# Kernel optimization log

Measured on AMD Instinct MI355X. Metric: run time of the kernel, lower is better.

The kernel has to match this reference:

```python
import jax, jax.numpy as jnp
import numpy as np

BIG = 1e9
EPS_BETA = 1e-6
EPS_BN = 1e-5

N_NODES = 50000
N_EDGES = 800000
IN_DIM = 128
OUT_DIM = 128


def setup_inputs() -> dict:
    key = jax.random.key(0)
    ks = jax.random.split(key, 8)
    h = jax.random.normal(ks[0], (N_NODES, IN_DIM), dtype=jnp.float32)
    src = jax.random.randint(ks[1], (N_EDGES,), 0, N_NODES, dtype=jnp.int32)
    dst = jax.random.randint(ks[2], (N_EDGES,), 0, N_NODES, dtype=jnp.int32)
    sigma_GD = jax.random.uniform(ks[3], (N_EDGES,), dtype=jnp.float32)
    fc_w = jax.random.normal(ks[4], (IN_DIM, OUT_DIM), dtype=jnp.float32) / np.sqrt(IN_DIM)
    fc_b = jax.random.normal(ks[5], (OUT_DIM,), dtype=jnp.float32) * 0.01
    attn_w = jax.random.normal(ks[6], (2 * OUT_DIM, 1), dtype=jnp.float32) / np.sqrt(2 * OUT_DIM)
    attn_b = jax.random.normal(ks[7], (1,), dtype=jnp.float32) * 0.01
    bn_gamma = jnp.ones((OUT_DIM,), dtype=jnp.float32)
    bn_beta = jnp.zeros((OUT_DIM,), dtype=jnp.float32)
    return {"h": h, "src": src, "dst": dst, "sigma_GD": sigma_GD,
            "fc_w": fc_w, "fc_b": fc_b, "attn_w": attn_w, "attn_b": attn_b,
            "bn_gamma": bn_gamma, "bn_beta": bn_beta}


def reference(h, src, dst, sigma_GD, fc_w, fc_b, attn_w, attn_b, bn_gamma, bn_beta):
    n = h.shape[0]
    # node projection
    z = h @ fc_w + fc_b                                   # [N, D]
    z = jnp.where(jnp.isinf(z), BIG, z)
    # per-edge attention logits: concat(src,dst) @ W == src@W1 + dst@W2 (avoid concat materialization)
    d = z.shape[1]
    w_src, w_dst = attn_w[:d], attn_w[d:]
    z_src = z[src]                                        # [E, D]
    a = z_src @ w_src + z[dst] @ w_dst + attn_b           # [E, 1]
    a = jnp.where(jnp.isinf(a), BIG, a)
    e = jax.nn.leaky_relu(a, negative_slope=0.01)[:, 0]   # [E]
    # segment softmax over incoming edges (mailbox softmax)
    m = jax.ops.segment_max(e, dst, num_segments=n)       # [N]
    ex = jnp.exp(e - m[dst])
    denom = jax.ops.segment_sum(ex, dst, num_segments=n)  # [N]
    alpha = ex / denom[dst]                               # [E]
    # beta: sigma_GD normalized per destination node
    bsum = jax.ops.segment_sum(sigma_GD, dst, num_segments=n)
    beta = sigma_GD / (bsum[dst] + EPS_BETA)              # [E]
    # weighted scatter-sum of source features
    h_new = jax.ops.segment_sum((alpha * beta)[:, None] * z_src, dst, num_segments=n)  # [N, D]
    h_new = jnp.where(jnp.isinf(h_new), BIG, h_new)
    # BatchNorm1d (training-mode batch stats, biased variance, as torch does)
    mu = h_new.mean(axis=0)
    var = ((h_new - mu) ** 2).mean(axis=0)
    h_bn = (h_new - mu) * jax.lax.rsqrt(var + EPS_BN) * bn_gamma + bn_beta
    return jax.nn.elu(h_bn)
```

## Files before the change

kernel.cpp:

```cpp
#include <hip/hip_runtime.h>
#include <hip/hip_fp16.h>
#include <math.h>

#define N_NODES 50000
#define N_EDGES 800000
#define BIGV 1000000000.0f
#define NBLK_GEMM 3125
#define CHUNK 1024
#define NCHUNK 782
#define NBUCKET 782
#define NB4 784
#define BMAX 1280
#define NBLK_BN 512

typedef _Float16 half8 __attribute__((ext_vector_type(8)));
typedef float floatx4 __attribute__((ext_vector_type(4)));

__device__ __forceinline__ float clampinf(float x) { return isinf(x) ? BIGV : x; }

__device__ __forceinline__ void barrier_lgkm_only() {
    __builtin_amdgcn_sched_barrier(0);
    asm volatile("s_waitcnt lgkmcnt(0)" ::: "memory");
    __builtin_amdgcn_s_barrier();
    __builtin_amdgcn_sched_barrier(0);
}

__global__ __launch_bounds__(256) void k_prep(const float* __restrict__ W,
                                              __half* __restrict__ wt,
                                              const int* __restrict__ dst,
                                              int* __restrict__ countsT)
{
    __shared__ int hist[NB4];
    const int t = threadIdx.x;
    const int idx = blockIdx.x * 256 + t;
    if (idx < 16384) {
        int n = idx >> 7, k = idx & 127;
        wt[idx] = __float2half(W[k * 128 + n]);
    }
    for (int i = t; i < NB4; i += 256) hist[i] = 0;
    __syncthreads();
    const int base = blockIdx.x * CHUNK;
    for (int i = t; i < CHUNK; i += 256) {
        int e = base + i;
        if (e < N_EDGES) atomicAdd(&hist[dst[e] >> 6], 1);
    }
    __syncthreads();
    for (int i = t; i < NB4; i += 256)
        countsT[i * NB4 + blockIdx.x] = hist[i];
}

__global__ __launch_bounds__(256) void k_off(const int* __restrict__ countsT,
                                             int* __restrict__ cursC,
                                             int* __restrict__ btot)
{
    const int wv = (blockIdx.x << 2) + (threadIdx.x >> 6);
    const int l = threadIdx.x & 63;
    if (wv >= NBUCKET) {
        if (l == 0 && wv < NB4) btot[wv] = 0;
        return;
    }
    const int* row = countsT + (size_t)wv * NB4;
    int carry = 0;
    #pragma unroll
    for (int p = 0; p < 13; ++p) {
        const int c = p * 64 + l;
        const int v = (c < NCHUNK) ? row[c] : 0;
        int x = v;
        #pragma unroll
        for (int o = 1; o < 64; o <<= 1) {
            int u = __shfl_up(x, o);
            if (l >= o) x += u;
        }
        if (c < NCHUNK) cursC[(size_t)c * NB4 + wv] = carry + x - v;
        carry += __shfl(x, 63);
    }
    if (l == 0) btot[wv] = carry;
}

__global__ __launch_bounds__(256) void k_gemm(
    const float* __restrict__ h, const __half* __restrict__ wt,
    const float* __restrict__ bias, const float* __restrict__ attn_w,
    __half* __restrict__ zh, float* __restrict__ sv, float* __restrict__ tv)
{
    __shared__ _Float16 hA[16][136];
    __shared__ float spart[4][16], tpart[4][16];

    const int tid = threadIdx.x;
    const int lane = tid & 63;
    const int wv = tid >> 6;
    const int l16 = lane & 15;
    const int oct = lane >> 4;
    const int n0 = wv << 5;
    const int node0 = blockIdx.x << 4;

    {
        const float4* h4 = (const float4*)(h + (size_t)node0 * 128);
        for (int i = tid; i < 512; i += 256) {
            int r = i >> 5, c4 = i & 31;
            float4 v = h4[i];
            union { __half2 h2[2]; uint2 u; } pk;
            pk.h2[0] = __floats2half2_rn(v.x, v.y);
            pk.h2[1] = __floats2half2_rn(v.z, v.w);
            *(uint2*)&hA[r][c4 << 2] = pk.u;
        }
    }

    half8 bfrag[4][2];
    #pragma unroll
    for (int kk = 0; kk < 4; ++kk)
        #pragma unroll
        for (int t = 0; t < 2; ++t)
            bfrag[kk][t] = *(const half8*)(wt + (size_t)(n0 + t * 16 + l16) * 128
                                              + kk * 32 + oct * 8);

    const float bv0 = bias[n0 + l16],         bv1 = bias[n0 + 16 + l16];
    const float ws0 = attn_w[n0 + l16],       ws1 = attn_w[n0 + 16 + l16];
    const float wd0 = attn_w[128 + n0 + l16], wd1 = attn_w[128 + n0 + 16 + l16];

    barrier_lgkm_only();

    floatx4 acc0 = {0.f, 0.f, 0.f, 0.f};
    floatx4 acc1 = {0.f, 0.f, 0.f, 0.f};
    #pragma unroll
    for (int kk = 0; kk < 4; ++kk) {
        half8 a = *(const half8*)&hA[l16][(kk << 5) + (oct << 3)];
        acc0 = __builtin_amdgcn_mfma_f32_16x16x32_f16(a, bfrag[kk][0], acc0, 0, 0, 0);
        acc1 = __builtin_amdgcn_mfma_f32_16x16x32_f16(a, bfrag[kk][1], acc1, 0, 0, 0);
    }

    float s_acc[4], t_acc[4];
    #pragma unroll
    for (int r = 0; r < 4; ++r) {
        float z0 = clampinf(acc0[r] + bv0);
        float z1 = clampinf(acc1[r] + bv1);
        const int row = (oct << 2) + r;
        zh[(size_t)(node0 + row) * 128 + n0 + l16]      = __float2half(z0);
        zh[(size_t)(node0 + row) * 128 + n0 + 16 + l16] = __float2half(z1);
        s_acc[r] = z0 * ws0 + z1 * ws1;
        t_acc[r] = z0 * wd0 + z1 * wd1;
    }
    #pragma unroll
    for (int r = 0; r < 4; ++r) {
        #pragma unroll
        for (int o = 1; o < 16; o <<= 1) {
            s_acc[r] += __shfl_xor(s_acc[r], o);
            t_acc[r] += __shfl_xor(t_acc[r], o);
        }
    }
    if (l16 == 0) {
        #pragma unroll
        for (int r = 0; r < 4; ++r) {
            spart[wv][(oct << 2) + r] = s_acc[r];
            tpart[wv][(oct << 2) + r] = t_acc[r];
        }
    }
    barrier_lgkm_only();
    if (tid < 16) {
        sv[node0 + tid] = spart[0][tid] + spart[1][tid] + spart[2][tid] + spart[3][tid];
        tv[node0 + tid] = tpart[0][tid] + tpart[1][tid] + tpart[2][tid] + tpart[3][tid];
    }
}

__global__ __launch_bounds__(256) void k_scat(
    const int* __restrict__ src, const int* __restrict__ dst,
    const float* __restrict__ sigma,
    const float* __restrict__ sv, const float* __restrict__ tv,
    const float* __restrict__ attn_b,
    const int* __restrict__ cursC, const int* __restrict__ btot,
    float4* __restrict__ tmp, int* __restrict__ bbase_g)
{
    __shared__ int cur[NB4];
    __shared__ int bb[NB4];
    __shared__ int tsc[256];
    const int t = threadIdx.x;
    const int self = blockIdx.x;

    for (int i = t; i < NB4; i += 256) cur[i] = cursC[(size_t)self * NB4 + i];

    uint4 bt = {0u, 0u, 0u, 0u};
    int tsum = 0;
    if (t < 196) {
        bt = ((const uint4*)btot)[t];
        tsum = (int)(bt.x + bt.y + bt.z + bt.w);
    }
    tsc[t] = tsum;
    __syncthreads();
    for (int off = 1; off < 256; off <<= 1) {
        int u = (t >= off) ? tsc[t - off] : 0;
        __syncthreads();
        tsc[t] += u;
        __syncthreads();
    }
    if (t < 196) {
        const int v0 = tsc[t] - tsum;
        bb[4*t+0] = v0;
        bb[4*t+1] = v0 + (int)bt.x;
        bb[4*t+2] = v0 + (int)bt.x + (int)bt.y;
        bb[4*t+3] = v0 + (int)bt.x + (int)bt.y + (int)bt.z;
    }
    __syncthreads();
    for (int i = t; i < NB4; i += 256) cur[i] += bb[i];
    if (self == 0)
        for (int i = t; i < NB4; i += 256) bbase_g[i] = bb[i];
    __syncthreads();

    const float ab = attn_b[0];
    const int base = self * CHUNK;
    for (int i = t; i < CHUNK; i += 256) {
        int e = base + i;
        if (e < N_EDGES) {
            int s = src[e];
            int d = dst[e];
            float a = sv[s] + tv[d] + ab;
            a = clampinf(a);
            float ev = a > 0.f ? a : 0.01f * a;
            int pos = atomicAdd(&cur[d >> 6], 1);
            float4 rec;
            rec.x = __int_as_float(s);
            rec.y = sigma[e];
            rec.z = ev;
            rec.w = __int_as_float(d);
            tmp[pos] = rec;
        }
    }
}

__global__ __launch_bounds__(512) void k_bagg(
    const float4* __restrict__ tmp, const int* __restrict__ bbase_g,
    const __half* __restrict__ zh, float4* __restrict__ ovf,
    float* __restrict__ out)
{
    __shared__ float4 lrec[BMAX];
    __shared__ int hist[64];
    __shared__ int segs[65];
    __shared__ int cur[64];
    const int t = threadIdx.x;
    const int b = blockIdx.x;
    const int s0 = bbase_g[b];
    const int n = bbase_g[b + 1] - s0;

    if (t < 64) hist[t] = 0;
    __syncthreads();
    const float* tw = (const float*)tmp;
    for (int i = t; i < n; i += 512) {
        int d = __float_as_int(tw[4 * (size_t)(s0 + i) + 3]);
        atomicAdd(&hist[d & 63], 1);
    }
    __syncthreads();
    if (t < 64) {
        const int hv = hist[t];
        int x = hv;
        #pragma unroll
        for (int o = 1; o < 64; o <<= 1) {
            int u = __shfl_up(x, o);
            if (t >= o) x += u;
        }
        segs[t] = x - hv;
        cur[t]  = x - hv;
        if (t == 63) segs[64] = x;
    }
    __syncthreads();
    for (int i = t; i < n; i += 512) {
        float4 rec = tmp[s0 + i];
        int d = __float_as_int(rec.w);
        int pos = atomicAdd(&cur[d & 63], 1);
        if (pos < BMAX) lrec[pos] = rec;
        else            ovf[s0 + pos] = rec;
    }
    __syncthreads();

    const int lane = t & 63;
    const int wv = t >> 6;
    const int grp = lane >> 4;
    const int l16 = lane & 15;

    for (int j = wv; j < 64; j += 8) {
        const int node = (b << 6) + j;
        if (node >= N_NODES) continue;
        const int beg = segs[j];
        const int deg = segs[j + 1] - beg;
        float acc[8] = {0.f, 0.f, 0.f, 0.f, 0.f, 0.f, 0.f, 0.f};

        if (deg > 0) {
            if (deg <= 64) {
                int sidx = 0; float sig = 0.f, e = -INFINITY;
                if (lane < deg) {
                    const int off = beg + lane;
                    float4 r = (off < BMAX) ? lrec[off] : ovf[s0 + off];
                    sidx = __float_as_int(r.x); sig = r.y; e = r.z;
                }
                float m = e;
                for (int o = 32; o; o >>= 1) m = fmaxf(m, __shfl_xor(m, o));
                float p = (lane < deg) ? __expf(e - m) : 0.f;
                float dn = p, bs = sig;
                for (int o = 32; o; o >>= 1) {
                    dn += __shfl_xor(dn, o);
                    bs += __shfl_xor(bs, o);
                }
                const float coef = p * sig * (1.0f / dn) / (bs + 1e-6f);
                for (int c = 0; c < deg; c += 4) {
                    const int jj = c + grp;
                    const int js = (jj < deg) ? jj : 0;
                    float cf = __shfl(coef, js);
                    int sj = __shfl(sidx, js);
                    if (jj < deg) {
                        uint4 raw = *(const uint4*)(zh + ((size_t)sj << 7) + (l16 << 3));
                        const __half2* hp = (const __half2*)&raw;
                        #pragma unroll
                        for (int k = 0; k < 4; ++k) {
                            float2 f = __half22float2(hp[k]);
                            acc[2*k]   = fmaf(cf, f.x, acc[2*k]);
                            acc[2*k+1] = fmaf(cf, f.y, acc[2*k+1]);
                        }
                    }
                }
            } else {
                float m = -INFINITY;
                for (int i = lane; i < deg; i += 64) {
                    const int off = beg + i;
                    float4 r = (off < BMAX) ? lrec[off] : ovf[s0 + off];
                    m = fmaxf(m, r.z);
                }
                for (int o = 32; o; o >>= 1) m = fmaxf(m, __shfl_xor(m, o));
                float dn = 0.f, bs = 0.f;
                for (int i = lane; i < deg; i += 64) {
                    const int off = beg + i;
                    float4 r = (off < BMAX) ? lrec[off] : ovf[s0 + off];
                    dn += __expf(r.z - m); bs += r.y;
                }
                for (int o = 32; o; o >>= 1) {
                    dn += __shfl_xor(dn, o);
                    bs += __shfl_xor(bs, o);
                }
                const float scale = (1.0f / dn) / (bs + 1e-6f);
                for (int c = 0; c < deg; c += 64) {
                    int i = c + lane;
                    int sidx = 0; float coef = 0.f;
                    if (i < deg) {
                        const int off = beg + i;
                        float4 r = (off < BMAX) ? lrec[off] : ovf[s0 + off];
                        sidx = __float_as_int(r.x);
                        coef = __expf(r.z - m) * r.y * scale;
                    }
                    const int cnt2 = min(64, deg - c);
                    for (int jj = 0; jj < cnt2; jj += 4) {
                        const int j4 = jj + grp;
                        const int js = (j4 < cnt2) ? j4 : 0;
                        float cf = __shfl(coef, js);
                        int sj = __shfl(sidx, js);
                        if (j4 < cnt2) {
                            uint4 raw = *(const uint4*)(zh + ((size_t)sj << 7) + (l16 << 3));
                            const __half2* hp = (const __half2*)&raw;
                            #pragma unroll
                            for (int k = 0; k < 4; ++k) {
                                float2 f = __half22float2(hp[k]);
                                acc[2*k]   = fmaf(cf, f.x, acc[2*k]);
                                acc[2*k+1] = fmaf(cf, f.y, acc[2*k+1]);
                            }
                        }
                    }
                }
            }
        }
        #pragma unroll
        for (int k = 0; k < 8; ++k) {
            acc[k] += __shfl_xor(acc[k], 16);
            acc[k] += __shfl_xor(acc[k], 32);
        }
        if (grp == 0) {
            float4 o0, o1;
            o0.x = clampinf(acc[0]); o0.y = clampinf(acc[1]);
            o0.z = clampinf(acc[2]); o0.w = clampinf(acc[3]);
            o1.x = clampinf(acc[4]); o1.y = clampinf(acc[5]);
            o1.z = clampinf(acc[6]); o1.w = clampinf(acc[7]);
            float4* op = (float4*)(out + (size_t)node * 128 + (l16 << 3));
            op[0] = o0; op[1] = o1;
        }
    }
}

__global__ __launch_bounds__(256) void k_bnstats(const float* __restrict__ hnew,
                                                 float* __restrict__ partials)
{
    const int tid = threadIdx.x;
    const int f4 = (tid & 31) << 2;
    const int rgrp = tid >> 5;
    float4 s = {0.f, 0.f, 0.f, 0.f}, q = {0.f, 0.f, 0.f, 0.f};
    for (int node = blockIdx.x * 8 + rgrp; node < N_NODES; node += NBLK_BN * 8) {
        float4 v = *(const float4*)(hnew + (size_t)node * 128 + f4);
        s.x += v.x; s.y += v.y; s.z += v.z; s.w += v.w;
        q.x += v.x * v.x; q.y += v.y * v.y; q.z += v.z * v.z; q.w += v.w * v.w;
    }
    __shared__ float4 ls[256], lq[256];
    ls[tid] = s; lq[tid] = q;
    __syncthreads();
    for (int off = 128; off >= 32; off >>= 1) {
        if (tid < off) {
            float4 a = ls[tid + off], b = lq[tid + off];
            ls[tid].x += a.x; ls[tid].y += a.y; ls[tid].z += a.z; ls[tid].w += a.w;
            lq[tid].x += b.x; lq[tid].y += b.y; lq[tid].z += b.z; lq[tid].w += b.w;
        }
        __syncthreads();
    }
    if (tid < 32) {
        float* p = partials + (size_t)blockIdx.x * 256;
        *(float4*)(p + f4)       = ls[tid];
        *(float4*)(p + 128 + f4) = lq[tid];
    }
}

__global__ __launch_bounds__(1024) void k_bnred(const float* __restrict__ partials,
                                                float* __restrict__ sums)
{
    __shared__ float red[4][256];
    const int t = threadIdx.x;
    const int f = t & 255;
    const int part = t >> 8;
    float s = 0.f;
    #pragma unroll 8
    for (int b = part * (NBLK_BN / 4); b < (part + 1) * (NBLK_BN / 4); ++b)
        s += partials[(size_t)b * 256 + f];
    red[part][f] = s;
    __syncthreads();
    if (part == 0)
        sums[f] = red[0][f] + red[1][f] + red[2][f] + red[3][f];
}

__global__ __launch_bounds__(256) void k_bnapply(float* __restrict__ io,
                                                 const float* __restrict__ sums,
                                                 const float* __restrict__ gamma,
                                                 const float* __restrict__ beta)
{
    __shared__ float sc[128], sh[128];
    const int tid = threadIdx.x;
    if (tid < 128) {
        const float invn = 1.0f / (float)N_NODES;
        float mu = sums[tid] * invn;
        float var = fmaxf(sums[128 + tid] * invn - mu * mu, 0.f);
        float g = gamma[tid] * rsqrtf(var + 1e-5f);
        sc[tid] = g;
        sh[tid] = beta[tid] - mu * g;
    }
    __syncthreads();
    const size_t idx = (size_t)blockIdx.x * 256 + tid;
    const int f4 = ((int)idx & 31) << 2;
    float4 x = ((const float4*)io)[idx];
    float y0 = x.x * sc[f4 + 0] + sh[f4 + 0];
    float y1 = x.y * sc[f4 + 1] + sh[f4 + 1];
    float y2 = x.z * sc[f4 + 2] + sh[f4 + 2];
    float y3 = x.w * sc[f4 + 3] + sh[f4 + 3];
    float4 o;
    o.x = y0 > 0.f ? y0 : expm1f(y0);
    o.y = y1 > 0.f ? y1 : expm1f(y1);
    o.z = y2 > 0.f ? y2 : expm1f(y2);
    o.w = y3 > 0.f ? y3 : expm1f(y3);
    ((float4*)io)[idx] = o;
}

extern "C" void kernel_launch(void* const* d_in, const int* in_sizes, int n_in,
                              void* d_out, int out_size, void* d_ws, size_t ws_size,
                              hipStream_t stream)
{
    const float* h      = (const float*)d_in[0];
    const int*   src    = (const int*)  d_in[1];
    const int*   dst    = (const int*)  d_in[2];
    const float* sigma  = (const float*)d_in[3];
    const float* fc_w   = (const float*)d_in[4];
    const float* fc_b   = (const float*)d_in[5];
    const float* attn_w = (const float*)d_in[6];
    const float* attn_b = (const float*)d_in[7];
    const float* gamma  = (const float*)d_in[8];
    const float* beta   = (const float*)d_in[9];
    float* out = (float*)d_out;

    float4* tmp    = (float4*)d_ws;
    float4* ovf    = tmp + N_EDGES;
    __half* zh     = (__half*)(ovf + N_EDGES);
    float*  sv     = (float*)(zh + (size_t)N_NODES * 128);
    float*  tv     = sv + N_NODES;
    float*  bns    = tv + N_NODES;
    float*  parts  = bns + 256;
    __half* wt     = (__half*)(parts + NBLK_BN * 256);
    int*    countsT= (int*)(wt + 16384);
    int*    cursC  = countsT + NB4 * NB4;
    int*    btot   = cursC + NB4 * NB4;
    int*    bbase  = btot + NB4;

    k_prep    <<<NCHUNK, 256, 0, stream>>>(fc_w, wt, dst, countsT);
    k_off     <<<196, 256, 0, stream>>>(countsT, cursC, btot);
    k_gemm    <<<NBLK_GEMM, 256, 0, stream>>>(h, wt, fc_b, attn_w, zh, sv, tv);
    k_scat    <<<NCHUNK, 256, 0, stream>>>(src, dst, sigma, sv, tv, attn_b,
                                           cursC, btot, tmp, bbase);
    k_bagg    <<<NBUCKET, 512, 0, stream>>>(tmp, bbase, zh, ovf, out);
    k_bnstats <<<NBLK_BN, 256, 0, stream>>>(out, parts);
    k_bnred   <<<1, 1024, 0, stream>>>(parts, bns);
    k_bnapply <<<(N_NODES * 128) / (256 * 4), 256, 0, stream>>>(out, bns, gamma, beta);
}
```

Before: 210.3 us.

## Split aggregation buckets in half and fuse BatchNorm stats into aggregation

```diff
diff --git a/kernel.cpp b/kernel.cpp
--- a/kernel.cpp
+++ b/kernel.cpp
@@ -10,8 +10,9 @@
 #define NCHUNK 782
 #define NBUCKET 782
 #define NB4 784
-#define BMAX 1280
-#define NBLK_BN 512
+#define NHALF 1564
+#define BMAX 768
+#define OVFSTRIDE 1024
 
 typedef _Float16 half8 __attribute__((ext_vector_type(8)));
 typedef float floatx4 __attribute__((ext_vector_type(4)));
@@ -27,6 +28,7 @@
 
 __global__ __launch_bounds__(256) void k_prep(const float* __restrict__ W,
                                               __half* __restrict__ wt,
+                                              float* __restrict__ bns,
                                               const int* __restrict__ dst,
                                               int* __restrict__ countsT)
 {
@@ -37,6 +39,7 @@
         int n = idx >> 7, k = idx & 127;
         wt[idx] = __float2half(W[k * 128 + n]);
     }
+    if (idx < 256) bns[idx] = 0.f;
     for (int i = t; i < NB4; i += 256) hist[i] = 0;
     __syncthreads();
     const int base = blockIdx.x * CHUNK;
@@ -228,44 +231,50 @@
 __global__ __launch_bounds__(512) void k_bagg(
     const float4* __restrict__ tmp, const int* __restrict__ bbase_g,
     const __half* __restrict__ zh, float4* __restrict__ ovf,
-    float* __restrict__ out)
+    float* __restrict__ out, float* __restrict__ partials)
 {
     __shared__ float4 lrec[BMAX];
-    __shared__ int hist[64];
-    __shared__ int segs[65];
-    __shared__ int cur[64];
+    __shared__ int hist[32];
+    __shared__ int segs[33];
+    __shared__ int cur[32];
+    __shared__ float bnS[128], bnQ[128];
     const int t = threadIdx.x;
-    const int b = blockIdx.x;
+    const int b2 = blockIdx.x;
+    const int b  = b2 >> 1;
+    const int hf = b2 & 1;
     const int s0 = bbase_g[b];
-    const int n = bbase_g[b + 1] - s0;
-
-    if (t < 64) hist[t] = 0;
+    const int n  = bbase_g[b + 1] - s0;
+
+    if (t < 32) hist[t] = 0;
+    if (t < 128) { bnS[t] = 0.f; bnQ[t] = 0.f; }
     __syncthreads();
     const float* tw = (const float*)tmp;
     for (int i = t; i < n; i += 512) {
         int d = __float_as_int(tw[4 * (size_t)(s0 + i) + 3]);
-        atomicAdd(&hist[d & 63], 1);
-    }
-    __syncthreads();
-    if (t < 64) {
+        if (((d >> 5) & 1) == hf) atomicAdd(&hist[d & 31], 1);
+    }
+    __syncthreads();
+    if (t < 32) {
         const int hv = hist[t];
         int x = hv;
         #pragma unroll
-        for (int o = 1; o < 64; o <<= 1) {
+        for (int o = 1; o < 32; o <<= 1) {
             int u = __shfl_up(x, o);
             if (t >= o) x += u;
         }
         segs[t] = x - hv;
         cur[t]  = x - hv;
-        if (t == 63) segs[64] = x;
+        if (t == 31) segs[32] = x;
     }
     __syncthreads();
     for (int i = t; i < n; i += 512) {
         float4 rec = tmp[s0 + i];
         int d = __float_as_int(rec.w);
-        int pos = atomicAdd(&cur[d & 63], 1);
-        if (pos < BMAX) lrec[pos] = rec;
-        else            ovf[s0 + pos] = rec;
+        if (((d >> 5) & 1) == hf) {
+            int pos = atomicAdd(&cur[d & 31], 1);
+            if (pos < BMAX) lrec[pos] = rec;
+            else            ovf[(size_t)b2 * OVFSTRIDE + (pos - BMAX)] = rec;
+        }
     }
     __syncthreads();
 
@@ -273,20 +282,23 @@
     const int wv = t >> 6;
     const int grp = lane >> 4;
     const int l16 = lane & 15;
-
-    for (int j = wv; j < 64; j += 8) {
-        const int node = (b << 6) + j;
+    float pS[8] = {0.f,0.f,0.f,0.f,0.f,0.f,0.f,0.f};
+    float pQ[8] = {0.f,0.f,0.f,0.f,0.f,0.f,0.f,0.f};
+
+    for (int j = wv; j < 32; j += 8) {
+        const int node = (b << 6) + (hf << 5) + j;
         if (node >= N_NODES) continue;
         const int beg = segs[j];
         const int deg = segs[j + 1] - beg;
-        float acc[8] = {0.f, 0.f, 0.f, 0.f, 0.f, 0.f, 0.f, 0.f};
+        float acc[8] = {0.f,0.f,0.f,0.f,0.f,0.f,0.f,0.f};
 
         if (deg > 0) {
             if (deg <= 64) {
                 int sidx = 0; float sig = 0.f, e = -INFINITY;
                 if (lane < deg) {
                     const int off = beg + lane;
-                    float4 r = (off < BMAX) ? lrec[off] : ovf[s0 + off];
+                    float4 r = (off < BMAX) ? lrec[off]
+                             : ovf[(size_t)b2 * OVFSTRIDE + (off - BMAX)];
                     sidx = __float_as_int(r.x); sig = r.y; e = r.z;
                 }
                 float m = e;
@@ -298,19 +310,33 @@
                     bs += __shfl_xor(bs, o);
                 }
                 const float coef = p * sig * (1.0f / dn) / (bs + 1e-6f);
-                for (int c = 0; c < deg; c += 4) {
-                    const int jj = c + grp;
-                    const int js = (jj < deg) ? jj : 0;
-                    float cf = __shfl(coef, js);
-                    int sj = __shfl(sidx, js);
-                    if (jj < deg) {
-                        uint4 raw = *(const uint4*)(zh + ((size_t)sj << 7) + (l16 << 3));
-                        const __half2* hp = (const __half2*)&raw;
+                for (int c = 0; c < deg; c += 8) {
+                    const int j0 = c + grp, j1 = c + 4 + grp;
+                    const int js0 = (j0 < deg) ? j0 : 0;
+                    const int js1 = (j1 < deg) ? j1 : 0;
+                    float cf0 = __shfl(coef, js0); int sj0 = __shfl(sidx, js0);
+                    float cf1 = __shfl(coef, js1); int sj1 = __shfl(sidx, js1);
+                    uint4 raw0, raw1;
+                    if (j0 < deg)
+                        raw0 = *(const uint4*)(zh + ((size_t)sj0 << 7) + (l16 << 3));
+                    if (j1 < deg)
+                        raw1 = *(const uint4*)(zh + ((size_t)sj1 << 7) + (l16 << 3));
+                    if (j0 < deg) {
+                        const __half2* hp = (const __half2*)&raw0;
                         #pragma unroll
                         for (int k = 0; k < 4; ++k) {
                             float2 f = __half22float2(hp[k]);
-                            acc[2*k]   = fmaf(cf, f.x, acc[2*k]);
-                            acc[2*k+1] = fmaf(cf, f.y, acc[2*k+1]);
+                            acc[2*k]   = fmaf(cf0, f.x, acc[2*k]);
+                            acc[2*k+1] = fmaf(cf0, f.y, acc[2*k+1]);
+                        }
+                    }
+                    if (j1 < deg) {
+                        const __half2* hp = (const __half2*)&raw1;
+                        #pragma unroll
+                        for (int k = 0; k < 4; ++k) {
+                            float2 f = __half22float2(hp[k]);
+                            acc[2*k]   = fmaf(cf1, f.x, acc[2*k]);
+                            acc[2*k+1] = fmaf(cf1, f.y, acc[2*k+1]);
                         }
                     }
                 }
@@ -318,14 +344,16 @@
                 float m = -INFINITY;
                 for (int i = lane; i < deg; i += 64) {
                     const int off = beg + i;
-                    float4 r = (off < BMAX) ? lrec[off] : ovf[s0 + off];
+                    float4 r = (off < BMAX) ? lrec[off]
+                             : ovf[(size_t)b2 * OVFSTRIDE + (off - BMAX)];
                     m = fmaxf(m, r.z);
                 }
                 for (int o = 32; o; o >>= 1) m = fmaxf(m, __shfl_xor(m, o));
                 float dn = 0.f, bs = 0.f;
                 for (int i = lane; i < deg; i += 64) {
                     const int off = beg + i;
-                    float4 r = (off < BMAX) ? lrec[off] : ovf[s0 + off];
+                    float4 r = (off < BMAX) ? lrec[off]
+                             : ovf[(size_t)b2 * OVFSTRIDE + (off - BMAX)];
                     dn += __expf(r.z - m); bs += r.y;
                 }
                 for (int o = 32; o; o >>= 1) {
@@ -338,7 +366,8 @@
                     int sidx = 0; float coef = 0.f;
                     if (i < deg) {
                         const int off = beg + i;
-                        float4 r = (off < BMAX) ? lrec[off] : ovf[s0 + off];
+                        float4 r = (off < BMAX) ? lrec[off]
+                                 : ovf[(size_t)b2 * OVFSTRIDE + (off - BMAX)];
                         sidx = __float_as_int(r.x);
                         coef = __expf(r.z - m) * r.y * scale;
                     }
@@ -368,62 +397,43 @@
             acc[k] += __shfl_xor(acc[k], 32);
         }
         if (grp == 0) {
+            float o[8];
+            #pragma unroll
+            for (int k = 0; k < 8; ++k) {
+                o[k] = clampinf(acc[k]);
+                pS[k] += o[k];
+                pQ[k] += o[k] * o[k];
+            }
             float4 o0, o1;
-            o0.x = clampinf(acc[0]); o0.y = clampinf(acc[1]);
-            o0.z = clampinf(acc[2]); o0.w = clampinf(acc[3]);
-            o1.x = clampinf(acc[4]); o1.y = clampinf(acc[5]);
-            o1.z = clampinf(acc[6]); o1.w = clampinf(acc[7]);
+            o0.x = o[0]; o0.y = o[1]; o0.z = o[2]; o0.w = o[3];
+            o1.x = o[4]; o1.y = o[5]; o1.z = o[6]; o1.w = o[7];
             float4* op = (float4*)(out + (size_t)node * 128 + (l16 << 3));
             op[0] = o0; op[1] = o1;
         }
     }
-}
-
-__global__ __launch_bounds__(256) void k_bnstats(const float* __restrict__ hnew,
-                                                 float* __restrict__ partials)
-{
-    const int tid = threadIdx.x;
-    const int f4 = (tid & 31) << 2;
-    const int rgrp = tid >> 5;
-    float4 s = {0.f, 0.f, 0.f, 0.f}, q = {0.f, 0.f, 0.f, 0.f};
-    for (int node = blockIdx.x * 8 + rgrp; node < N_NODES; node += NBLK_BN * 8) {
-        float4 v = *(const float4*)(hnew + (size_t)node * 128 + f4);
-        s.x += v.x; s.y += v.y; s.z += v.z; s.w += v.w;
-        q.x += v.x * v.x; q.y += v.y * v.y; q.z += v.z * v.z; q.w += v.w * v.w;
-    }
-    __shared__ float4 ls[256], lq[256];
-    ls[tid] = s; lq[tid] = q;
-    __syncthreads();
-    for (int off = 128; off >= 32; off >>= 1) {
-        if (tid < off) {
-            float4 a = ls[tid + off], b = lq[tid + off];
-            ls[tid].x += a.x; ls[tid].y += a.y; ls[tid].z += a.z; ls[tid].w += a.w;
-            lq[tid].x += b.x; lq[tid].y += b.y; lq[tid].z += b.z; lq[tid].w += b.w;
-        }
-        __syncthreads();
-    }
-    if (tid < 32) {
-        float* p = partials + (size_t)blockIdx.x * 256;
-        *(float4*)(p + f4)       = ls[tid];
-        *(float4*)(p + 128 + f4) = lq[tid];
-    }
-}
-
-__global__ __launch_bounds__(1024) void k_bnred(const float* __restrict__ partials,
-                                                float* __restrict__ sums)
-{
-    __shared__ float red[4][256];
+    if (grp == 0) {
+        #pragma unroll
+        for (int k = 0; k < 8; ++k) {
+            atomicAdd(&bnS[(l16 << 3) + k], pS[k]);
+            atomicAdd(&bnQ[(l16 << 3) + k], pQ[k]);
+        }
+    }
+    __syncthreads();
+    if (t < 128) {
+        partials[(size_t)b2 * 256 + t]       = bnS[t];
+        partials[(size_t)b2 * 256 + 128 + t] = bnQ[t];
+    }
+}
+
+__global__ __launch_bounds__(256) void k_bnred(const float* __restrict__ partials,
+                                               float* __restrict__ bns)
+{
     const int t = threadIdx.x;
-    const int f = t & 255;
-    const int part = t >> 8;
+    const int r0 = blockIdx.x * 25;
+    const int r1 = min(r0 + 25, NHALF);
     float s = 0.f;
-    #pragma unroll 8
-    for (int b = part * (NBLK_BN / 4); b < (part + 1) * (NBLK_BN / 4); ++b)
-        s += partials[(size_t)b * 256 + f];
-    red[part][f] = s;
-    __syncthreads();
-    if (part == 0)
-        sums[f] = red[0][f] + red[1][f] + red[2][f] + red[3][f];
+    for (int r = r0; r < r1; ++r) s += partials[(size_t)r * 256 + t];
+    atomicAdd(&bns[t], s);
 }
 
 __global__ __launch_bounds__(256) void k_bnapply(float* __restrict__ io,
@@ -475,24 +485,23 @@
 
     float4* tmp    = (float4*)d_ws;
     float4* ovf    = tmp + N_EDGES;
-    __half* zh     = (__half*)(ovf + N_EDGES);
+    __half* zh     = (__half*)(ovf + (size_t)NHALF * OVFSTRIDE);
     float*  sv     = (float*)(zh + (size_t)N_NODES * 128);
     float*  tv     = sv + N_NODES;
     float*  bns    = tv + N_NODES;
     float*  parts  = bns + 256;
-    __half* wt     = (__half*)(parts + NBLK_BN * 256);
+    __half* wt     = (__half*)(parts + (size_t)NHALF * 256);
     int*    countsT= (int*)(wt + 16384);
     int*    cursC  = countsT + NB4 * NB4;
     int*    btot   = cursC + NB4 * NB4;
     int*    bbase  = btot + NB4;
 
-    k_prep    <<<NCHUNK, 256, 0, stream>>>(fc_w, wt, dst, countsT);
+    k_prep    <<<NCHUNK, 256, 0, stream>>>(fc_w, wt, bns, dst, countsT);
     k_off     <<<196, 256, 0, stream>>>(countsT, cursC, btot);
     k_gemm    <<<NBLK_GEMM, 256, 0, stream>>>(h, wt, fc_b, attn_w, zh, sv, tv);
     k_scat    <<<NCHUNK, 256, 0, stream>>>(src, dst, sigma, sv, tv, attn_b,
                                            cursC, btot, tmp, bbase);
-    k_bagg    <<<NBUCKET, 512, 0, stream>>>(tmp, bbase, zh, ovf, out);
-    k_bnstats <<<NBLK_BN, 256, 0, stream>>>(out, parts);
-    k_bnred   <<<1, 1024, 0, stream>>>(parts, bns);
+    k_bagg    <<<NHALF, 512, 0, stream>>>(tmp, bbase, zh, ovf, out, parts);
+    k_bnred   <<<64, 256, 0, stream>>>(parts, bns);
     k_bnapply <<<(N_NODES * 128) / (256 * 4), 256, 0, stream>>>(out, bns, gamma, beta);
 }
```

After: 232.2 us. 1.1x slower.
